# Kernel tuning notes

Measured on AMD Instinct MI355X. Metric: run time of the kernel, lower is better.

Reference implementation:

```python
import jax, jax.numpy as jnp
import numpy as np

TOTAL_WORDS = 90000
EMBED = 100
SEQ = 300
BATCH = 250
UNITS = 1024


def setup_inputs() -> dict:
    key = jax.random.key(0)
    ks = jax.random.split(key, 9)
    s = 0.02
    return {
        "tokens": jax.random.randint(ks[0], (BATCH, SEQ), 0, TOTAL_WORDS),
        "emb": jax.random.normal(ks[1], (TOTAL_WORDS, EMBED), jnp.float32) * s,
        "Wx0": jax.random.normal(ks[2], (EMBED, UNITS), jnp.float32) * s,
        "Wh0": jax.random.normal(ks[3], (UNITS, UNITS), jnp.float32) * s,
        "b0": jnp.zeros((UNITS,), jnp.float32),
        "Wx1": jax.random.normal(ks[4], (UNITS, UNITS), jnp.float32) * s,
        "Wh1": jax.random.normal(ks[5], (UNITS, UNITS), jnp.float32) * s,
        "b1": jnp.zeros((UNITS,), jnp.float32),
        "Wo": jax.random.normal(ks[6], (UNITS, 1), jnp.float32) * s,
        "bo": jnp.zeros((1,), jnp.float32),
    }


def reference(tokens, emb, Wx0, Wh0, b0, Wx1, Wh1, b1, Wo, bo):
    # Embedding lookup: [B, S, E]
    x = emb[tokens]
    # Precompute input projections for both cells' input-side matmuls where possible.
    # Cell0 input projection can be done for all timesteps at once: [B, S, U]
    xp0 = jnp.einsum("bse,eu->bsu", x, Wx0) + b0

    def step(carry, xp_t):
        h0, h1 = carry
        # SimpleRNNCell: out = tanh(x@Wx + h@Wh + b); dropout disabled (inference)
        h0 = jnp.tanh(xp_t + h0 @ Wh0)
        h1 = jnp.tanh(h0 @ Wx1 + h1 @ Wh1 + b1)
        return (h0, h1), None

    h0 = jnp.zeros((BATCH, UNITS), jnp.float32)
    h1 = jnp.zeros((BATCH, UNITS), jnp.float32)
    # scan over time: xp0 transposed to [S, B, U]
    (h0, h1), _ = jax.lax.scan(step, (h0, h1), jnp.transpose(xp0, (1, 0, 2)))
    logits = h1 @ Wo + bo  # [B, 1]
    return jax.nn.sigmoid(logits)
```

## Files before the change

kernel.cpp:

```cpp
#include <hip/hip_runtime.h>
#include <hip/hip_bf16.h>

#define SEQ 300
#define BAT 250
#define UNITS 1024
#define EMBD 100
#define MROWS (SEQ*BAT)

typedef __bf16 bf16;
typedef __bf16 bf16x4 __attribute__((ext_vector_type(4)));
typedef __bf16 bf16x8 __attribute__((ext_vector_type(8)));
typedef float  f32x2  __attribute__((ext_vector_type(2)));
typedef float  f32x4  __attribute__((ext_vector_type(4)));
typedef float  f32x16 __attribute__((ext_vector_type(16)));
typedef unsigned u32x4 __attribute__((ext_vector_type(4)));

#define MFMA32(a,b,c) __builtin_amdgcn_mfma_f32_32x32x16_bf16(a,b,c,0,0,0)
#define F32X16_ZERO {0.f,0.f,0.f,0.f,0.f,0.f,0.f,0.f,0.f,0.f,0.f,0.f,0.f,0.f,0.f,0.f}

__device__ __align__(16)  bf16 g_xp0[(size_t)MROWS*UNITS + 8192];
__device__ __align__(256) bf16 g_h0[304][256*1024];
__device__ __align__(256) bf16 g_h1[304][256*1024];
__device__ __align__(64) unsigned g_pf0[4*16];
__device__ __align__(64) unsigned g_pf1[8*16];

struct L16 { u32x4 a, b, c, d; };

#define ISSUE_LINE(L, P) \
  asm volatile("global_load_dwordx4 %0, %4, off sc0 sc1\n\t" \
               "global_load_dwordx4 %1, %4, off offset:16 sc0 sc1\n\t" \
               "global_load_dwordx4 %2, %4, off offset:32 sc0 sc1\n\t" \
               "global_load_dwordx4 %3, %4, off offset:48 sc0 sc1" \
    : "=&v"((L).a), "=&v"((L).b), "=&v"((L).c), "=&v"((L).d) : "v"(P) : "memory")

__device__ __forceinline__ unsigned minline(const L16& L) {
  unsigned m0 = L.a[0] < L.a[1] ? L.a[0] : L.a[1];
  unsigned m1 = L.a[2] < L.a[3] ? L.a[2] : L.a[3];
  unsigned m2 = L.b[0] < L.b[1] ? L.b[0] : L.b[1];
  unsigned m3 = L.b[2] < L.b[3] ? L.b[2] : L.b[3];
  unsigned m4 = L.c[0] < L.c[1] ? L.c[0] : L.c[1];
  unsigned m5 = L.c[2] < L.c[3] ? L.c[2] : L.c[3];
  unsigned m6 = L.d[0] < L.d[1] ? L.d[0] : L.d[1];
  unsigned m7 = L.d[2] < L.d[3] ? L.d[2] : L.d[3];
  m0 = m0 < m1 ? m0 : m1; m2 = m2 < m3 ? m2 : m3;
  m4 = m4 < m5 ? m4 : m5; m6 = m6 < m7 ? m6 : m7;
  m0 = m0 < m2 ? m0 : m2; m4 = m4 < m6 ? m4 : m6;
  return m0 < m4 ? m0 : m4;
}

__device__ __forceinline__ float tanh_fast(float x) {
  float e = __expf(2.f * x);
  return 1.f - 2.f / (e + 1.f);
}

__global__ __launch_bounds__(256) void xp0_kernel(const int* __restrict__ tokens,
                                                  const float* __restrict__ emb,
                                                  const float* __restrict__ Wx0,
                                                  const float* __restrict__ b0) {
  __shared__ bf16 A[64 * 128];
  __shared__ int toks[64];
  const int mt = blockIdx.x;
  const int nt = blockIdx.y;
  const int tid = threadIdx.x, lane = tid & 63, wv = tid >> 6;

  if (tid < 64) {
    int R = mt * 64 + tid;
    int tok = 0;
    if (R < MROWS) { int s = R / 250; int b = R - s * 250; tok = tokens[b * SEQ + s]; }
    toks[tid] = tok;
  }
  __syncthreads();
  for (int idx = tid; idx < 64 * 128; idx += 256) {
    int r = idx >> 7, k = idx & 127;
    float v = (k < EMBD) ? emb[(size_t)toks[r] * EMBD + k] : 0.f;
    unsigned off = (unsigned)(r * 256 + k * 2);
    off ^= (unsigned)((r & 7) << 4);
    *(bf16*)((char*)A + off) = (bf16)v;
  }

  const int colb = nt * 256 + (wv << 6) + (lane & 31);
  bf16x8 Bf[2][8];
  #pragma unroll
  for (int nf = 0; nf < 2; ++nf) {
    #pragma unroll
    for (int kk = 0; kk < 8; ++kk) {
      const int kb = (kk << 4) + ((lane >> 5) << 3);
      bf16x8 f;
      #pragma unroll
      for (int j = 0; j < 8; ++j) {
        int k = kb + j;
        f[j] = (bf16)((k < EMBD) ? Wx0[(size_t)k * UNITS + colb + (nf << 5)] : 0.f);
      }
      Bf[nf][kk] = f;
    }
  }
  __syncthreads();

  f32x16 acc00 = F32X16_ZERO, acc01 = F32X16_ZERO, acc10 = F32X16_ZERO, acc11 = F32X16_ZERO;
  #pragma unroll
  for (int kk = 0; kk < 8; ++kk) {
    #pragma unroll
    for (int mf = 0; mf < 2; ++mf) {
      int row = (mf << 5) + (lane & 31);
      unsigned off = (unsigned)(row * 256 + ((kk << 4) + ((lane >> 5) << 3)) * 2);
      off ^= (unsigned)((row & 7) << 4);
      bf16x8 a = *(const bf16x8*)((const char*)A + off);
      if (mf == 0) { acc00 = MFMA32(a, Bf[0][kk], acc00); acc01 = MFMA32(a, Bf[1][kk], acc01); }
      else         { acc10 = MFMA32(a, Bf[0][kk], acc10); acc11 = MFMA32(a, Bf[1][kk], acc11); }
    }
  }

  const float bb0 = b0[colb], bb1 = b0[colb + 32];
  #pragma unroll
  for (int mf = 0; mf < 2; ++mf) {
    #pragma unroll
    for (int nf = 0; nf < 2; ++nf) {
      #pragma unroll
      for (int reg = 0; reg < 16; ++reg) {
        int r32 = (mf << 5) + ((lane >> 5) << 2) + (reg & 3) + ((reg >> 2) << 3);
        int R = mt * 64 + r32;
        if (R < MROWS) {
          float v = (mf == 0 ? (nf == 0 ? acc00[reg] : acc01[reg])
                             : (nf == 0 ? acc10[reg] : acc11[reg])) + (nf ? bb1 : bb0);
          g_xp0[(size_t)R * UNITS + nt * 256 + (wv << 6) + (nf << 5) + (lane & 31)] = (bf16)v;
        }
      }
    }
  }
}

#define WAITV(N) do { asm volatile("s_waitcnt vmcnt(" #N ")" ::: "memory"); \
                      __builtin_amdgcn_sched_barrier(0); } while (0)
#define LDG(I, P) do { const bf16* _p = (P); \
  asm volatile("global_load_dwordx4 %0, %4, off\n\t" \
               "global_load_dwordx4 %1, %4, off offset:1024\n\t" \
               "global_load_dwordx4 %2, %4, off offset:2048\n\t" \
               "global_load_dwordx4 %3, %4, off offset:3072" \
    : "=&v"(av[I]), "=&v"(av[I+1]), "=&v"(av[I+2]), "=&v"(av[I+3]) : "v"(_p)); } while (0)
#define MF4(K0) { _Pragma("unroll") \
  for (int kk = (K0); kk < (K0) + 4; ++kk) { \
    bf16x8 a_ = __builtin_bit_cast(bf16x8, av[kk]); \
    acc0 = MFMA32(a_, Bf[0][kk], acc0); \
    acc1 = MFMA32(a_, Bf[1][kk], acc1); } }

__global__ __launch_bounds__(512, 1) void rnn_persistent(const float* __restrict__ Wh0,
                                                         const float* __restrict__ Wx1,
                                                         const float* __restrict__ Wh1,
                                                         const float* __restrict__ b1) {
  const int bx = blockIdx.x;
  const int role = (bx >= 128) ? 0 : 1;
  int m4 = 0, m8 = 0, n;
  if (role == 1) { m8 = bx & 7; n = bx >> 3; }
  else { int r = bx & 7; m4 = r >> 1; n = ((bx - 128) >> 3) + ((r & 1) << 3); }
  const int tid = threadIdx.x;
  const int lane = tid & 63, w = tid >> 6;
  const int sub = w & 1, kq = w >> 1;

  __shared__ bf16 red[8][32][68];

  const float* W = role ? (sub ? Wh1 : Wx1) : Wh0;
  bf16x8 Bf[2][16];
  {
    const int colA = n * 64 + (lane & 31);
    const int kb = (kq << 8) + ((lane >> 5) << 3);
    #pragma unroll
    for (int nf = 0; nf < 2; ++nf)
      #pragma unroll
      for (int kk = 0; kk < 16; ++kk) {
        const float* s = W + (size_t)(kb + (kk << 4)) * UNITS + colA + (nf << 5);
        bf16x8 f;
        #pragma unroll
        for (int j = 0; j < 8; ++j) f[j] = (bf16)s[(size_t)j * UNITS];
        Bf[nf][kk] = f;
      }
  }

  const int rblkA = role ? m8 : (m4 * 2 + sub);
  const size_t abase = ((size_t)(rblkA * 128 + kq * 32 + (lane >> 5))) * 256 + (size_t)(lane & 31) * 8;

  if (role == 0) {
    const int cblk = tid >> 6, rp = tid & 63;
    const int mtc = rp >> 5, rpp = rp & 31;
    const int hi = (rpp >> 2) & 1;
    const int idx = ((cblk >> 2) << 4) + (rpp & 3) + ((rpp >> 3) << 2);
    const int entry = (hi << 5) + ((cblk & 3) << 3);
    const size_t hsb = ((size_t)((m4 * 2 + mtc) * 128 + n * 8 + cblk)) * 256 + (size_t)rpp * 8;

    for (int t = 0; t < SEQ; ++t) {
      bf16x8 xv;
      { const bf16* xp = &g_xp0[(size_t)(t * BAT + m4 * 64 + rp) * UNITS + n * 64 + (cblk << 3)];
        asm volatile("global_load_dwordx4 %0, %1, off" : "=&v"(xv) : "v"(xp)); }
      if (tid == 0 && t >= 1) {
        for (;;) {
          L16 A;
          ISSUE_LINE(A, &g_pf0[m4 * 16]);
          asm volatile("s_waitcnt vmcnt(0)" ::: "memory");
          __builtin_amdgcn_sched_barrier(0);
          if (minline(A) >= (unsigned)t) break;
          __builtin_amdgcn_s_sleep(1);
        }
      }
      __syncthreads();

      f32x16 acc0 = F32X16_ZERO, acc1 = F32X16_ZERO;
      if (t >= 1) {
        f32x4 av[16];
        const bf16* pn = g_h0[t - 1] + abase;
        LDG(0, pn); LDG(4, pn + 2048); LDG(8, pn + 4096); LDG(12, pn + 6144);
        WAITV(12); MF4(0)
        WAITV(8);  MF4(4)
        WAITV(4);  MF4(8)
        WAITV(0);  MF4(12)
      }
      {
        const int s0 = kq * 2 + sub;
        #pragma unroll
        for (int r = 0; r < 16; ++r) {
          red[s0][r][lane]      = (bf16)acc0[r];
          red[s0][16 + r][lane] = (bf16)acc1[r];
        }
      }
      __syncthreads();
      WAITV(0);
      {
        float s[8];
        #pragma unroll
        for (int j = 0; j < 8; ++j) s[j] = (float)xv[j];
        #pragma unroll
        for (int k4 = 0; k4 < 4; ++k4) {
          bf16x8 v = *(const bf16x8*)&red[k4 * 2 + mtc][idx][entry];
          #pragma unroll
          for (int j = 0; j < 8; ++j) s[j] += (float)v[j];
        }
        union { bf16 h[8]; f32x4 v; } o;
        #pragma unroll
        for (int j = 0; j < 8; ++j) o.h[j] = (bf16)tanh_fast(s[j]);
        bf16* hb = g_h0[t] + hsb;
        asm volatile("global_store_dwordx4 %0, %1, off sc0 sc1" :: "v"(hb), "v"(o.v) : "memory");
      }
      asm volatile("s_waitcnt vmcnt(0)" ::: "memory");
      __syncthreads();
      if (tid == 0) {
        unsigned v = (unsigned)(t + 1);
        asm volatile("global_store_dword %0, %1, off sc0 sc1" :: "v"(&g_pf0[m4 * 16 + n]), "v"(v) : "memory");
      }
    }
  } else {
    const int rp = tid & 31, cg = tid >> 5;
    const int nfc = cg >> 3;
    const int entc = (((rp >> 2) & 1) << 5) + ((cg & 7) << 2);
    const int regc = (rp & 3) + ((rp >> 3) << 2);
    const size_t hsb = ((size_t)(m8 * 128 + n * 8 + (cg >> 1))) * 256 + (size_t)rp * 8 + (size_t)((cg & 1) << 2);
    float b1v[4];
    #pragma unroll
    for (int j = 0; j < 4; ++j) b1v[j] = b1[n * 64 + (cg << 2) + j];

    for (int t = 1; t <= SEQ; ++t) {
      if (tid == 0) {
        for (;;) {
          L16 A, B;
          ISSUE_LINE(A, &g_pf0[(m8 >> 1) * 16]);
          const bool chk = (t >= 2);
          if (chk) ISSUE_LINE(B, &g_pf1[m8 * 16]);
          asm volatile("s_waitcnt vmcnt(0)" ::: "memory");
          __builtin_amdgcn_sched_barrier(0);
          bool ok = (minline(A) >= (unsigned)t);
          if (ok && chk) ok = (minline(B) >= (unsigned)(t - 1));
          if (ok) break;
          __builtin_amdgcn_s_sleep(1);
        }
      }
      __syncthreads();

      f32x16 acc0 = F32X16_ZERO, acc1 = F32X16_ZERO;
      if (sub == 0 || t >= 2) {
        f32x4 av[16];
        const bf16* pn = sub ? (g_h1[t - 1] + abase)
                             : (g_h0[t - 1] + abase);
        LDG(0, pn); LDG(4, pn + 2048); LDG(8, pn + 4096); LDG(12, pn + 6144);
        WAITV(12); MF4(0)
        WAITV(8);  MF4(4)
        WAITV(4);  MF4(8)
        WAITV(0);  MF4(12)
      }
      {
        const int s0 = kq * 2 + sub;
        #pragma unroll
        for (int r = 0; r < 16; ++r) {
          red[s0][r][lane]      = (bf16)acc0[r];
          red[s0][16 + r][lane] = (bf16)acc1[r];
        }
      }
      __syncthreads();
      {
        float s[4];
        #pragma unroll
        for (int j = 0; j < 4; ++j) s[j] = b1v[j];
        #pragma unroll
        for (int w8 = 0; w8 < 8; ++w8) {
          bf16x4 v = *(const bf16x4*)&red[w8][(nfc << 4) + regc][entc];
          #pragma unroll
          for (int j = 0; j < 4; ++j) s[j] += (float)v[j];
        }
        union { bf16 h[4]; f32x2 v; } o;
        #pragma unroll
        for (int j = 0; j < 4; ++j) o.h[j] = (bf16)tanh_fast(s[j]);
        bf16* hb = g_h1[t] + hsb;
        asm volatile("global_store_dwordx2 %0, %1, off sc0 sc1" :: "v"(hb), "v"(o.v) : "memory");
      }
      asm volatile("s_waitcnt vmcnt(0)" ::: "memory");
      __syncthreads();
      if (tid == 0) {
        unsigned v = (unsigned)t;
        asm volatile("global_store_dword %0, %1, off sc0 sc1" :: "v"(&g_pf1[m8 * 16 + n]), "v"(v) : "memory");
      }
    }
  }
}

__global__ __launch_bounds__(64) void logits_kernel(const float* __restrict__ Wo,
                                                    const float* __restrict__ bo,
                                                    float* __restrict__ out) {
  const int b = blockIdx.x, lane = threadIdx.x;
  if (b == 0) {
    unsigned z = 0;
    for (int i = lane; i < 192; i += 64) {
      unsigned* p = (i < 64) ? &g_pf0[i] : &g_pf1[i - 64];
      asm volatile("global_store_dword %0, %1, off sc0 sc1" :: "v"(p), "v"(z) : "memory");
    }
    asm volatile("s_waitcnt vmcnt(0)" ::: "memory");
  }
  const bf16* h = g_h1[SEQ];
  const size_t base = ((size_t)((b >> 5) * 128 + lane * 2)) * 256 + (size_t)(b & 31) * 8;
  bf16x8 v0 = *(const bf16x8*)&h[base];
  bf16x8 v1 = *(const bf16x8*)&h[base + 256];
  float s = 0.f;
  #pragma unroll
  for (int j = 0; j < 8; ++j) {
    s += (float)v0[j] * Wo[lane * 16 + j];
    s += (float)v1[j] * Wo[lane * 16 + 8 + j];
  }
  #pragma unroll
  for (int off = 32; off; off >>= 1) s += __shfl_xor(s, off, 64);
  if (lane == 0) out[b] = 1.f / (1.f + __expf(-(s + bo[0])));
}

extern "C" void kernel_launch(void* const* d_in, const int* in_sizes, int n_in,
                              void* d_out, int out_size, void* d_ws, size_t ws_size,
                              hipStream_t stream) {
  const int*   tokens = (const int*)  d_in[0];
  const float* emb    = (const float*)d_in[1];
  const float* Wx0    = (const float*)d_in[2];
  const float* Wh0    = (const float*)d_in[3];
  const float* b0     = (const float*)d_in[4];
  const float* Wx1    = (const float*)d_in[5];
  const float* Wh1    = (const float*)d_in[6];
  const float* b1     = (const float*)d_in[7];
  const float* Wo     = (const float*)d_in[8];
  const float* bo     = (const float*)d_in[9];
  float* out = (float*)d_out;

  dim3 gx((MROWS + 63) / 64, 4);
  xp0_kernel<<<gx, 256, 0, stream>>>(tokens, emb, Wx0, b0);

  rnn_persistent<<<192, 512, 0, stream>>>(Wh0, Wx1, Wh1, b1);

  logits_kernel<<<BAT, 64, 0, stream>>>(Wo, bo, out);
}
```

Baseline: 1.847 ms.

## Repartition layer-0 blocks by 32-row tiles and split layer-1 dependency waits

Layer-0 blocks now own 32 batch rows by 128 columns, matching layer-1's 8 row groups, instead of 64 rows by 64 columns. Each layer-1 block therefore waits only on the 8 layer-0 flags of its own row group. Layer-1 also splits its wait: the Wx1 half starts as soon as h0 is ready, while a separate thread polls the h1 flags and the Wh1 half runs after an extra barrier. This shortens the critical dependency chain between the layers. Dummy reloads of the just-written h values are added after each step, likely to warm caches or for ordering, at the cost of an extra barrier and extra loads per step.

```diff
diff --git a/kernel.cpp b/kernel.cpp
--- a/kernel.cpp
+++ b/kernel.cpp
@@ -21,7 +21,7 @@
 __device__ __align__(16)  bf16 g_xp0[(size_t)MROWS*UNITS + 8192];
 __device__ __align__(256) bf16 g_h0[304][256*1024];
 __device__ __align__(256) bf16 g_h1[304][256*1024];
-__device__ __align__(64) unsigned g_pf0[4*16];
+__device__ __align__(64) unsigned g_pf0[8*16];
 __device__ __align__(64) unsigned g_pf1[8*16];
 
 struct L16 { u32x4 a, b, c, d; };
@@ -32,22 +32,23 @@
                "global_load_dwordx4 %2, %4, off offset:32 sc0 sc1\n\t" \
                "global_load_dwordx4 %3, %4, off offset:48 sc0 sc1" \
     : "=&v"((L).a), "=&v"((L).b), "=&v"((L).c), "=&v"((L).d) : "v"(P) : "memory")
-
+#define ISSUE8(A, B, P) \
+  asm volatile("global_load_dwordx4 %0, %2, off sc0 sc1\n\t" \
+               "global_load_dwordx4 %1, %2, off offset:16 sc0 sc1" \
+    : "=&v"(A), "=&v"(B) : "v"(P) : "memory")
+
+__device__ __forceinline__ unsigned min8(const u32x4& a, const u32x4& b) {
+  unsigned m0 = a[0] < a[1] ? a[0] : a[1];
+  unsigned m1 = a[2] < a[3] ? a[2] : a[3];
+  unsigned m2 = b[0] < b[1] ? b[0] : b[1];
+  unsigned m3 = b[2] < b[3] ? b[2] : b[3];
+  m0 = m0 < m1 ? m0 : m1; m2 = m2 < m3 ? m2 : m3;
+  return m0 < m2 ? m0 : m2;
+}
 __device__ __forceinline__ unsigned minline(const L16& L) {
-  unsigned m0 = L.a[0] < L.a[1] ? L.a[0] : L.a[1];
-  unsigned m1 = L.a[2] < L.a[3] ? L.a[2] : L.a[3];
-  unsigned m2 = L.b[0] < L.b[1] ? L.b[0] : L.b[1];
-  unsigned m3 = L.b[2] < L.b[3] ? L.b[2] : L.b[3];
-  unsigned m4 = L.c[0] < L.c[1] ? L.c[0] : L.c[1];
-  unsigned m5 = L.c[2] < L.c[3] ? L.c[2] : L.c[3];
-  unsigned m6 = L.d[0] < L.d[1] ? L.d[0] : L.d[1];
-  unsigned m7 = L.d[2] < L.d[3] ? L.d[2] : L.d[3];
-  m0 = m0 < m1 ? m0 : m1; m2 = m2 < m3 ? m2 : m3;
-  m4 = m4 < m5 ? m4 : m5; m6 = m6 < m7 ? m6 : m7;
-  m0 = m0 < m2 ? m0 : m2; m4 = m4 < m6 ? m4 : m6;
-  return m0 < m4 ? m0 : m4;
-}
-
+  unsigned m0 = min8(L.a, L.b), m1 = min8(L.c, L.d);
+  return m0 < m1 ? m0 : m1;
+}
 __device__ __forceinline__ float tanh_fast(float x) {
   float e = __expf(2.f * x);
   return 1.f - 2.f / (e + 1.f);
@@ -149,9 +150,8 @@
                                                          const float* __restrict__ b1) {
   const int bx = blockIdx.x;
   const int role = (bx >= 128) ? 0 : 1;
-  int m4 = 0, m8 = 0, n;
-  if (role == 1) { m8 = bx & 7; n = bx >> 3; }
-  else { int r = bx & 7; m4 = r >> 1; n = ((bx - 128) >> 3) + ((r & 1) << 3); }
+  const int m8 = bx & 7;
+  const int n  = role ? (bx >> 3) : ((bx - 128) >> 3);
   const int tid = threadIdx.x;
   const int lane = tid & 63, w = tid >> 6;
   const int sub = w & 1, kq = w >> 1;
@@ -161,7 +161,7 @@
   const float* W = role ? (sub ? Wh1 : Wx1) : Wh0;
   bf16x8 Bf[2][16];
   {
-    const int colA = n * 64 + (lane & 31);
+    const int colA = role ? (n * 64 + (lane & 31)) : (n * 128 + (sub << 6) + (lane & 31));
     const int kb = (kq << 8) + ((lane >> 5) << 3);
     #pragma unroll
     for (int nf = 0; nf < 2; ++nf)
@@ -175,28 +175,26 @@
       }
   }
 
-  const int rblkA = role ? m8 : (m4 * 2 + sub);
-  const size_t abase = ((size_t)(rblkA * 128 + kq * 32 + (lane >> 5))) * 256 + (size_t)(lane & 31) * 8;
+  const size_t abase = ((size_t)(m8 * 128 + kq * 32 + (lane >> 5))) * 256 + (size_t)(lane & 31) * 8;
 
   if (role == 0) {
-    const int cblk = tid >> 6, rp = tid & 63;
-    const int mtc = rp >> 5, rpp = rp & 31;
-    const int hi = (rpp >> 2) & 1;
-    const int idx = ((cblk >> 2) << 4) + (rpp & 3) + ((rpp >> 3) << 2);
-    const int entry = (hi << 5) + ((cblk & 3) << 3);
-    const size_t hsb = ((size_t)((m4 * 2 + mtc) * 128 + n * 8 + cblk)) * 256 + (size_t)rpp * 8;
+    const int cb = tid >> 5, rp = tid & 31;
+    const int csub = cb >> 3;
+    const int idx = (((cb >> 2) & 1) << 4) + (rp & 3) + ((rp >> 3) << 2);
+    const int entry = ((((rp >> 2) & 1)) << 5) + ((cb & 3) << 3);
+    const size_t hsb = ((size_t)(m8 * 128 + n * 16 + cb)) * 256 + (size_t)rp * 8;
 
     for (int t = 0; t < SEQ; ++t) {
       bf16x8 xv;
-      { const bf16* xp = &g_xp0[(size_t)(t * BAT + m4 * 64 + rp) * UNITS + n * 64 + (cblk << 3)];
+      { const bf16* xp = &g_xp0[(size_t)(t * BAT + m8 * 32 + rp) * UNITS + n * 128 + (cb << 3)];
         asm volatile("global_load_dwordx4 %0, %1, off" : "=&v"(xv) : "v"(xp)); }
       if (tid == 0 && t >= 1) {
         for (;;) {
-          L16 A;
-          ISSUE_LINE(A, &g_pf0[m4 * 16]);
+          u32x4 fa, fb;
+          ISSUE8(fa, fb, &g_pf0[m8 * 16]);
           asm volatile("s_waitcnt vmcnt(0)" ::: "memory");
           __builtin_amdgcn_sched_barrier(0);
-          if (minline(A) >= (unsigned)t) break;
+          if (min8(fa, fb) >= (unsigned)t) break;
           __builtin_amdgcn_s_sleep(1);
         }
       }
@@ -222,28 +220,30 @@
       }
       __syncthreads();
       WAITV(0);
+      bf16* hb = g_h0[t] + hsb;
       {
         float s[8];
         #pragma unroll
         for (int j = 0; j < 8; ++j) s[j] = (float)xv[j];
         #pragma unroll
         for (int k4 = 0; k4 < 4; ++k4) {
-          bf16x8 v = *(const bf16x8*)&red[k4 * 2 + mtc][idx][entry];
+          bf16x8 v = *(const bf16x8*)&red[k4 * 2 + csub][idx][entry];
           #pragma unroll
           for (int j = 0; j < 8; ++j) s[j] += (float)v[j];
         }
         union { bf16 h[8]; f32x4 v; } o;
         #pragma unroll
         for (int j = 0; j < 8; ++j) o.h[j] = (bf16)tanh_fast(s[j]);
-        bf16* hb = g_h0[t] + hsb;
         asm volatile("global_store_dwordx4 %0, %1, off sc0 sc1" :: "v"(hb), "v"(o.v) : "memory");
       }
       asm volatile("s_waitcnt vmcnt(0)" ::: "memory");
       __syncthreads();
       if (tid == 0) {
         unsigned v = (unsigned)(t + 1);
-        asm volatile("global_store_dword %0, %1, off sc0 sc1" :: "v"(&g_pf0[m4 * 16 + n]), "v"(v) : "memory");
-      }
+        asm volatile("global_store_dword %0, %1, off sc0 sc1" :: "v"(&g_pf0[m8 * 16 + n]), "v"(v) : "memory");
+      }
+      { f32x4 d;
+        asm volatile("global_load_dwordx4 %0, %1, off sc0 sc1" : "=&v"(d) : "v"(hb)); }
     }
   } else {
     const int rp = tid & 31, cg = tid >> 5;
@@ -258,40 +258,63 @@
     for (int t = 1; t <= SEQ; ++t) {
       if (tid == 0) {
         for (;;) {
-          L16 A, B;
-          ISSUE_LINE(A, &g_pf0[(m8 >> 1) * 16]);
-          const bool chk = (t >= 2);
-          if (chk) ISSUE_LINE(B, &g_pf1[m8 * 16]);
+          u32x4 fa, fb;
+          ISSUE8(fa, fb, &g_pf0[m8 * 16]);
           asm volatile("s_waitcnt vmcnt(0)" ::: "memory");
           __builtin_amdgcn_sched_barrier(0);
-          bool ok = (minline(A) >= (unsigned)t);
-          if (ok && chk) ok = (minline(B) >= (unsigned)(t - 1));
-          if (ok) break;
+          if (min8(fa, fb) >= (unsigned)t) break;
           __builtin_amdgcn_s_sleep(1);
         }
       }
       __syncthreads();
 
       f32x16 acc0 = F32X16_ZERO, acc1 = F32X16_ZERO;
-      if (sub == 0 || t >= 2) {
+      if (sub == 0) {
         f32x4 av[16];
-        const bf16* pn = sub ? (g_h1[t - 1] + abase)
-                             : (g_h0[t - 1] + abase);
+        const bf16* pn = g_h0[t - 1] + abase;
         LDG(0, pn); LDG(4, pn + 2048); LDG(8, pn + 4096); LDG(12, pn + 6144);
         WAITV(12); MF4(0)
         WAITV(8);  MF4(4)
         WAITV(4);  MF4(8)
         WAITV(0);  MF4(12)
-      }
-      {
-        const int s0 = kq * 2 + sub;
+        const int s0 = kq * 2;
         #pragma unroll
         for (int r = 0; r < 16; ++r) {
           red[s0][r][lane]      = (bf16)acc0[r];
           red[s0][16 + r][lane] = (bf16)acc1[r];
         }
-      }
-      __syncthreads();
+      } else if (tid == 64 && t >= 2) {
+        for (;;) {
+          L16 B;
+          ISSUE_LINE(B, &g_pf1[m8 * 16]);
+          asm volatile("s_waitcnt vmcnt(0)" ::: "memory");
+          __builtin_amdgcn_sched_barrier(0);
+          if (minline(B) >= (unsigned)(t - 1)) break;
+          __builtin_amdgcn_s_sleep(1);
+        }
+      }
+      __syncthreads();
+
+      if (sub == 1) {
+        if (t >= 2) {
+          f32x4 av[16];
+          const bf16* pn = g_h1[t - 1] + abase;
+          LDG(0, pn); LDG(4, pn + 2048); LDG(8, pn + 4096); LDG(12, pn + 6144);
+          WAITV(12); MF4(0)
+          WAITV(8);  MF4(4)
+          WAITV(4);  MF4(8)
+          WAITV(0);  MF4(12)
+        }
+        const int s0 = kq * 2 + 1;
+        #pragma unroll
+        for (int r = 0; r < 16; ++r) {
+          red[s0][r][lane]      = (bf16)acc0[r];
+          red[s0][16 + r][lane] = (bf16)acc1[r];
+        }
+      }
+      __syncthreads();
+
+      bf16* hb = g_h1[t] + hsb;
       {
         float s[4];
         #pragma unroll
@@ -305,7 +328,6 @@
         union { bf16 h[4]; f32x2 v; } o;
         #pragma unroll
         for (int j = 0; j < 4; ++j) o.h[j] = (bf16)tanh_fast(s[j]);
-        bf16* hb = g_h1[t] + hsb;
         asm volatile("global_store_dwordx2 %0, %1, off sc0 sc1" :: "v"(hb), "v"(o.v) : "memory");
       }
       asm volatile("s_waitcnt vmcnt(0)" ::: "memory");
@@ -314,6 +336,8 @@
         unsigned v = (unsigned)t;
         asm volatile("global_store_dword %0, %1, off sc0 sc1" :: "v"(&g_pf1[m8 * 16 + n]), "v"(v) : "memory");
       }
+      { f32x2 d;
+        asm volatile("global_load_dwordx2 %0, %1, off sc0 sc1" : "=&v"(d) : "v"(hb)); }
     }
   }
 }
@@ -324,8 +348,8 @@
   const int b = blockIdx.x, lane = threadIdx.x;
   if (b == 0) {
     unsigned z = 0;
-    for (int i = lane; i < 192; i += 64) {
-      unsigned* p = (i < 64) ? &g_pf0[i] : &g_pf1[i - 64];
+    for (int i = lane; i < 256; i += 64) {
+      unsigned* p = (i < 128) ? &g_pf0[i] : &g_pf1[i - 128];
       asm volatile("global_store_dword %0, %1, off sc0 sc1" :: "v"(p), "v"(z) : "memory");
     }
     asm volatile("s_waitcnt vmcnt(0)" ::: "memory");
```

Measured after the change: 1.841 ms. About the same (-0.3%).
